# Performance work log

Measured on AMD Instinct MI355X. Metric: run time of the kernel, lower is better.

## Reference

```python
import jax, jax.numpy as jnp
import numpy as np

NUM_HEADS = 16
D_MODEL = 1024
DK = D_MODEL // NUM_HEADS


def setup_inputs() -> dict:
    key = jax.random.key(0)
    kH, kq, kk, kv, ko = jax.random.split(key, 5)
    scale = 0.02
    return {
        "H": jax.random.normal(kH, (4, 2048, D_MODEL), dtype=jnp.float32),
        "Wq": jax.random.normal(kq, (D_MODEL, D_MODEL), dtype=jnp.float32) * scale,
        "Wk": jax.random.normal(kk, (D_MODEL, D_MODEL), dtype=jnp.float32) * scale,
        "Wv": jax.random.normal(kv, (D_MODEL, D_MODEL), dtype=jnp.float32) * scale,
        "Wo": jax.random.normal(ko, (D_MODEL, D_MODEL), dtype=jnp.float32) * scale,
    }


def reference(H, Wq, Wk, Wv, Wo):
    b, T, d = H.shape
    n, dk = NUM_HEADS, DK
    # projections -> [b, n, T, dk]
    def split_heads(x):
        return x.reshape(b, T, n, dk).transpose(0, 2, 1, 3)
    Q = split_heads(H @ Wq)
    K = split_heads(H @ Wk)
    V = split_heads(H @ Wv)
    scores = jnp.einsum("bntd,bnsd->bnts", Q, K) / jnp.sqrt(jnp.float32(dk))
    causal = jnp.tril(jnp.ones((T, T), dtype=bool))
    scores = jnp.where(causal[None, None], scores, -jnp.inf)
    attn = jax.nn.softmax(scores, axis=-1)  # dropout rate 0 -> identity
    out = jnp.einsum("bnts,bnsd->bntd", attn, V)  # [b, n, T, dk]
    out = out.transpose(0, 2, 1, 3).reshape(b, T, n * dk)
    return out @ Wo
```

## Files before the change

### kernel.cpp

```cpp
#include <hip/hip_runtime.h>
#include <hip/hip_bf16.h>

#define T_SEQ 2048
#define DM 1024
#define DM2 2048
#define NH 16
#define DKH 64
#define NBATCH 4
#define MROWS (NBATCH*T_SEQ)

typedef __attribute__((ext_vector_type(8))) short bf16x8;
typedef __attribute__((ext_vector_type(4))) short bf16x4;
typedef __attribute__((ext_vector_type(4))) float f32x4;
typedef __attribute__((ext_vector_type(4))) unsigned short u16x4;

#define NEG_INF (-__builtin_inff())

#if __has_builtin(__builtin_amdgcn_exp2f)
#define EXP2(x) __builtin_amdgcn_exp2f(x)
#else
#define EXP2(x) exp2f(x)
#endif

static __device__ __forceinline__ unsigned short f2bf(float f){
  union { float f; unsigned u; } v; v.f = f;
  unsigned r = v.u + 0x7fffu + ((v.u >> 16) & 1u);
  return (unsigned short)(r >> 16);
}

static __device__ __forceinline__ unsigned short f2bfc(float f){
  union { __hip_bfloat16 h; unsigned short u; } cv;
  cv.h = __float2bfloat16(f);
  return cv.u;
}

static __device__ __forceinline__ void gload_lds16(const void* g, void* l){
  __builtin_amdgcn_global_load_lds(
      (const __attribute__((address_space(1))) void*)g,
      (__attribute__((address_space(3))) void*)l, 16, 0, 0);
}

__global__ __launch_bounds__(256) void convprep(
    const float* __restrict__ H,
    const float* __restrict__ W0, const float* __restrict__ W1,
    const float* __restrict__ W2, const float* __restrict__ W3,
    u16x4* __restrict__ Hb4,
    unsigned short* __restrict__ O0, unsigned short* __restrict__ O1,
    unsigned short* __restrict__ O2, unsigned short* __restrict__ O3)
{
  __shared__ float t[32][33];
  const int bid = blockIdx.x, tid = threadIdx.x;
  if (bid < 4096){
    const int z = bid >> 10, rem = bid & 1023;
    const int nx = (rem & 31)*32, kx = (rem >> 5)*32;
    const float* W = (z==0)?W0:(z==1)?W1:(z==2)?W2:W3;
    unsigned short* O = (z==0)?O0:(z==1)?O1:(z==2)?O2:O3;
    const float sc = (z==0) ? 0.18033688f : 1.0f;
    const int tx = tid & 31, ty = tid >> 5;
    #pragma unroll
    for (int i = 0; i < 4; ++i)
      t[ty + i*8][tx] = W[(size_t)(kx + ty + i*8)*DM + nx + tx];
    __syncthreads();
    #pragma unroll
    for (int i = 0; i < 4; ++i)
      O[(size_t)(nx + ty + i*8)*DM + kx + tx] = f2bf(t[tx][ty + i*8] * sc);
  } else {
    const int n4 = MROWS*DM/4;
    for (int i = (bid - 4096)*256 + tid; i < n4; i += 2048*256){
      float4 v = ((const float4*)H)[i];
      u16x4 o;
      o[0] = f2bf(v.x); o[1] = f2bf(v.y); o[2] = f2bf(v.z); o[3] = f2bf(v.w);
      Hb4[i] = o;
    }
  }
}

template<bool F32OUT>
static __device__ __forceinline__ void gemm_body(
    const unsigned short* __restrict__ A, const unsigned short* __restrict__ Bt,
    void* __restrict__ Cp, int N, int K, int m0, int n0,
    unsigned short* a_lds, unsigned short* b_lds)
{
  const int tid = threadIdx.x;
  const int w = tid >> 6, l = tid & 63;
  const int g = l >> 4, lr = l & 15;
  const int wr = w >> 1, wc = w & 1;
  f32x4 acc[4][4] = {};
  const int nk = K >> 6;
  for (int ks = 0; ks < nk; ++ks){
    __syncthreads();
    const int k0 = ks << 6;
    #pragma unroll
    for (int i = 0; i < 4; ++i){
      int c = (w*4 + i)*64 + l;
      int row = c >> 3;
      int gc = (c & 7) ^ (row & 7);
      gload_lds16(A + (size_t)(m0 + row)*K + (k0 + gc*8), &a_lds[c*8]);
    }
    #pragma unroll
    for (int i = 0; i < 4; ++i){
      int c = (w*4 + i)*64 + l;
      int row = c >> 3;
      int gc = (c & 7) ^ (row & 7);
      gload_lds16(Bt + (size_t)(n0 + row)*K + (k0 + gc*8), &b_lds[c*8]);
    }
    __syncthreads();
    #pragma unroll
    for (int kc = 0; kc < 2; ++kc){
      bf16x8 af[4], bf_[4];
      #pragma unroll
      for (int mt = 0; mt < 4; ++mt){
        int row = wr*64 + mt*16 + lr;
        int off = row*128 + ((kc*64 + g*16) ^ ((row & 7) << 4));
        af[mt] = *(const bf16x8*)((const char*)a_lds + off);
      }
      #pragma unroll
      for (int nt = 0; nt < 4; ++nt){
        int row = wc*64 + nt*16 + lr;
        int off = row*128 + ((kc*64 + g*16) ^ ((row & 7) << 4));
        bf_[nt] = *(const bf16x8*)((const char*)b_lds + off);
      }
      #pragma unroll
      for (int mt = 0; mt < 4; ++mt)
        #pragma unroll
        for (int nt = 0; nt < 4; ++nt)
          acc[mt][nt] = __builtin_amdgcn_mfma_f32_16x16x32_bf16(af[mt], bf_[nt], acc[mt][nt], 0, 0, 0);
    }
  }
  #pragma unroll
  for (int mt = 0; mt < 4; ++mt){
    #pragma unroll
    for (int nt = 0; nt < 4; ++nt){
      const int col = n0 + wc*64 + nt*16 + lr;
      #pragma unroll
      for (int r = 0; r < 4; ++r){
        const int row = m0 + wr*64 + mt*16 + 4*g + r;
        if (F32OUT) ((float*)Cp)[(size_t)row*N + col] = acc[mt][nt][r];
        else ((unsigned short*)Cp)[(size_t)row*N + col] = f2bf(acc[mt][nt][r]);
      }
    }
  }
}

__global__ __launch_bounds__(256) void gemm_qkv(
    const unsigned short* __restrict__ Hb, const unsigned short* __restrict__ Wqkt,
    unsigned short* __restrict__ QKb,
    const unsigned short* __restrict__ Wvt, unsigned short* __restrict__ Vtb)
{
  __shared__ __attribute__((aligned(16))) unsigned short a_lds[128*64];
  __shared__ __attribute__((aligned(16))) unsigned short b_lds[128*64];
  const int bid = blockIdx.x;
  const unsigned short *A, *Bt; unsigned short* Cp; int N, m0, n0;
  if (bid < 1024){
    A = Hb; Bt = Wqkt; Cp = QKb; N = DM2;
    m0 = (bid & 63)*128; n0 = (bid >> 6)*128;
  } else {
    const int t2 = bid - 1024;
    A = Wvt; Bt = Hb; Cp = Vtb; N = MROWS;
    m0 = (t2 & 7)*128; n0 = (t2 >> 3)*128;
  }
  gemm_body<false>(A, Bt, Cp, N, DM, m0, n0, a_lds, b_lds);
}

__global__ __launch_bounds__(256) void gemm_out(
    const unsigned short* __restrict__ Ab, const unsigned short* __restrict__ Wot,
    float* __restrict__ Out)
{
  __shared__ __attribute__((aligned(16))) unsigned short a_lds[128*64];
  __shared__ __attribute__((aligned(16))) unsigned short b_lds[128*64];
  gemm_body<true>(Ab, Wot, Out, DM, DM, blockIdx.x*128, blockIdx.y*128, a_lds, b_lds);
}

static __device__ __forceinline__ void softmax_tile8(
    f32x4 (&s)[8], float& m_run, f32x4 (&acc)[5],
    bf16x4 (&pb)[8], int j0, int qg, int g, bool fullTile)
{
  if (!fullTile){
    #pragma unroll
    for (int kc = 0; kc < 8; ++kc)
      #pragma unroll
      for (int r = 0; r < 4; ++r){
        int kvg = j0 + kc*16 + 4*g + r;
        s[kc][r] = (kvg <= qg) ? s[kc][r] : NEG_INF;
      }
  }
  float m4[8];
  #pragma unroll
  for (int kc = 0; kc < 8; ++kc)
    m4[kc] = fmaxf(fmaxf(s[kc][0], s[kc][1]), fmaxf(s[kc][2], s[kc][3]));
  float tm = fmaxf(fmaxf(fmaxf(m4[0], m4[1]), fmaxf(m4[2], m4[3])),
                   fmaxf(fmaxf(m4[4], m4[5]), fmaxf(m4[6], m4[7])));
  tm = fmaxf(tm, __shfl_xor(tm, 16));
  tm = fmaxf(tm, __shfl_xor(tm, 32));
  float mm;
  if (__all(tm - m_run <= 8.f)){
    mm = m_run;
  } else {
    const float m_new = fmaxf(m_run, tm);
    const float fac = EXP2(m_run - m_new);
    m_run = m_new; mm = m_new;
    #pragma unroll
    for (int mt = 0; mt < 5; ++mt){
      acc[mt][0] *= fac; acc[mt][1] *= fac; acc[mt][2] *= fac; acc[mt][3] *= fac;
    }
  }
  #pragma unroll
  for (int kc = 0; kc < 8; ++kc){
    float e0 = EXP2(s[kc][0] - mm); float e1 = EXP2(s[kc][1] - mm);
    float e2 = EXP2(s[kc][2] - mm); float e3 = EXP2(s[kc][3] - mm);
    bf16x4 t;
    t[0] = (short)f2bfc(e0); t[1] = (short)f2bfc(e1);
    t[2] = (short)f2bfc(e2); t[3] = (short)f2bfc(e3);
    pb[kc] = t;
  }
}

__global__ __launch_bounds__(512, 4) void attn_kernel(const unsigned short* __restrict__ QK,
                                                      const unsigned short* __restrict__ Vt,
                                                      unsigned short* __restrict__ Og)
{
  __shared__ __attribute__((aligned(16))) unsigned short k_lds[2][128*64];
  __shared__ __attribute__((aligned(16))) unsigned short v_lds[2][64*128];
  const int tid = threadIdx.x;
  const int w = tid >> 6, l = tid & 63;
  const int g = l >> 4, lr = l & 15;
  const int L = blockIdx.x;
  const int xcd = L & 7, idx = L >> 3;
  const int bh = xcd*8 + (idx & 7);
  const int pair = idx >> 3;
  const int b = bh >> 4, h = bh & 15;
  const size_t baseK = (size_t)(b*T_SEQ)*DM2 + 1024 + h*DKH;
  const size_t baseV = (size_t)(h*DKH)*MROWS + (size_t)b*T_SEQ;
  const bf16x4 vone = {(short)0x3F80, (short)0x3F80, (short)0x3F80, (short)0x3F80};

  const int cA = tid, cB = tid + 512;
  const int krA = cA >> 3, kgA = (cA & 7) ^ (krA & 7);
  const int krB = cB >> 3, kgB = (cB & 7) ^ (krB & 7);
  const int vrA = cA >> 4, vgA = (cA & 15) ^ (vrA & 15);
  const int vrB = cB >> 4, vgB = (cB & 15) ^ (vrB & 15);

  auto STAGE = [&](int jt, int buf){
    const int j0s = jt * 128;
    gload_lds16(QK + baseK + (size_t)(j0s + krA)*DM2 + kgA*8, &k_lds[buf][cA*8]);
    gload_lds16(QK + baseK + (size_t)(j0s + krB)*DM2 + kgB*8, &k_lds[buf][cB*8]);
    gload_lds16(Vt + baseV + (size_t)vrA*MROWS + j0s + vgA*8, &v_lds[buf][cA*8]);
    gload_lds16(Vt + baseV + (size_t)vrB*MROWS + j0s + vgB*8, &v_lds[buf][cB*8]);
  };

#define ROUND(JT, CUR) do{                                                       \
    const int jt_ = (JT);                                                        \
    if (jt_ + 1 < ntiles) STAGE(jt_ + 1, (CUR)^1);                               \
    const int j0_ = jt_ * 128;                                                   \
    f32x4 s[8];                                                                  \
    __builtin_amdgcn_s_setprio(1);                                               \
    _Pragma("unroll")                                                            \
    for (int kc = 0; kc < 8; ++kc){                                              \
      f32x4 z = {};                                                              \
      _Pragma("unroll")                                                          \
      for (int c2 = 0; c2 < 2; ++c2){                                            \
        int row = kc*16 + lr;                                                    \
        int off = row*128 + ((c2*64 + g*16) ^ ((row & 7) << 4));                 \
        bf16x8 kf = *(const bf16x8*)((const char*)k_lds[CUR] + off);             \
        z = __builtin_amdgcn_mfma_f32_16x16x32_bf16(kf, qf[c2], z, 0, 0, 0);     \
      }                                                                          \
      s[kc] = z;                                                                 \
    }                                                                            \
    __builtin_amdgcn_s_setprio(0);                                               \
    bf16x4 pb[8];                                                                \
    softmax_tile8(s, m_run, acc, pb, j0_, qg, g, jt_ < qblk);                    \
    __builtin_amdgcn_s_setprio(1);                                               \
    _Pragma("unroll")                                                            \
    for (int mt = 0; mt < 4; ++mt){                                              \
      const int vrow = mt*16 + lr;                                               \
      _Pragma("unroll")                                                          \
      for (int kc = 0; kc < 8; ++kc){                                            \
        const int voff = vrow*256 + ((((kc<<1) + (g>>1)) ^ (vrow & 15)) << 4)    \
                         + ((g & 1) << 3);                                       \
        bf16x4 vf = *(const bf16x4*)((const char*)v_lds[CUR] + voff);            \
        acc[mt] = __builtin_amdgcn_mfma_f32_16x16x16bf16_1k(vf, pb[kc], acc[mt], 0, 0, 0); \
      }                                                                          \
    }                                                                            \
    _Pragma("unroll")                                                            \
    for (int kc = 0; kc < 8; ++kc)                                               \
      acc[4] = __builtin_amdgcn_mfma_f32_16x16x16bf16_1k(vone, pb[kc], acc[4], 0, 0, 0); \
    __builtin_amdgcn_s_setprio(0);                                               \
    __syncthreads();                                                             \
  } while(0)

  #pragma unroll 1
  for (int seg = 0; seg < 2; ++seg){
    const int qblk = seg ? pair : (15 - pair);
    const int q0 = qblk * 128;
    const int qg = q0 + w*16 + lr;
    const size_t rowQ = (size_t)(b*T_SEQ + qg)*DM2 + h*DKH;
    bf16x8 qf[2];
    qf[0] = *(const bf16x8*)(QK + rowQ + g*8);
    qf[1] = *(const bf16x8*)(QK + rowQ + 32 + g*8);
    float m_run = NEG_INF;
    f32x4 acc[5] = {};
    const int ntiles = qblk + 1;

    STAGE(0, 0);
    __syncthreads();

    int jt = 0;
    #pragma unroll 1
    for (; jt + 2 <= ntiles; jt += 2){
      ROUND(jt, 0);
      ROUND(jt + 1, 1);
    }
    if (jt < ntiles) ROUND(jt, 0);

    const float inv = 1.f / acc[4][0];
    const size_t rowO = (size_t)(b*T_SEQ + qg)*DM + h*DKH;
    #pragma unroll
    for (int mt = 0; mt < 4; ++mt){
      unsigned u0 = (unsigned)f2bfc(acc[mt][0]*inv) | ((unsigned)f2bfc(acc[mt][1]*inv) << 16);
      unsigned u1 = (unsigned)f2bfc(acc[mt][2]*inv) | ((unsigned)f2bfc(acc[mt][3]*inv) << 16);
      *(unsigned*)(Og + rowO + mt*16 + 4*g)     = u0;
      *(unsigned*)(Og + rowO + mt*16 + 4*g + 2) = u1;
    }
  }
#undef ROUND
}

extern "C" void kernel_launch(void* const* d_in, const int* in_sizes, int n_in,
                              void* d_out, int out_size, void* d_ws, size_t ws_size,
                              hipStream_t stream)
{
  (void)in_sizes; (void)n_in; (void)out_size; (void)ws_size;
  const float* H  = (const float*)d_in[0];
  const float* Wq = (const float*)d_in[1];
  const float* Wk = (const float*)d_in[2];
  const float* Wv = (const float*)d_in[3];
  const float* Wo = (const float*)d_in[4];
  char* ws = (char*)d_ws;
  unsigned short* Hb   = (unsigned short*)(ws);
  unsigned short* Wqkt = (unsigned short*)(ws + 16777216);
  unsigned short* Wkt  = (unsigned short*)(ws + 18874368);
  unsigned short* Wvt  = (unsigned short*)(ws + 20971520);
  unsigned short* Wot  = (unsigned short*)(ws + 23068672);
  unsigned short* QKb  = (unsigned short*)(ws + 25165824);
  unsigned short* Vtb  = (unsigned short*)(ws + 58720256);
  unsigned short* Ab   = (unsigned short*)(ws + 75497472);

  convprep<<<6144, 256, 0, stream>>>(H, Wq, Wk, Wv, Wo,
                                     (u16x4*)Hb, Wqkt, Wkt, Wvt, Wot);
  gemm_qkv<<<1536, 256, 0, stream>>>(Hb, Wqkt, QKb, Wvt, Vtb);
  attn_kernel<<<dim3(512), 512, 0, stream>>>(QKb, Vtb, Ab);
  gemm_out<<<dim3(64,8), 256, 0, stream>>>(Ab, Wot, (float*)d_out);
}
```

Baseline: 171.2 us.

## Rewrite attention kernel with 32x32 MFMA tiles and 256-row query blocks

Switches the attention kernel from 16x16 MFMA tiles to 32x32x16 bf16 MFMA. Each wave now owns 32 query rows and each block covers 256 query rows, so the grid halves to 256 blocks and launch bounds drop to 2 blocks per CU. The row sum is now kept in a scalar accumulator instead of an extra ones-vector MFMA, and causal half-tiles beyond a wave's rows are skipped. K rows are permuted at staging time to match the 32x32 output layout. The goal is fewer MFMA and LDS instructions per FLOP, at the cost of lower occupancy, a smaller grid, and more register pressure.

```diff
diff --git a/kernel.cpp b/kernel.cpp
--- a/kernel.cpp
+++ b/kernel.cpp
@@ -12,6 +12,7 @@
 typedef __attribute__((ext_vector_type(8))) short bf16x8;
 typedef __attribute__((ext_vector_type(4))) short bf16x4;
 typedef __attribute__((ext_vector_type(4))) float f32x4;
+typedef __attribute__((ext_vector_type(16))) float f32x16;
 typedef __attribute__((ext_vector_type(4))) unsigned short u16x4;
 
 #define NEG_INF (-__builtin_inff())
@@ -21,6 +22,8 @@
 #else
 #define EXP2(x) exp2f(x)
 #endif
+
+#define MFMA32(A,B,C) __builtin_amdgcn_mfma_f32_32x32x16_bf16(A,B,C,0,0,0)
 
 static __device__ __forceinline__ unsigned short f2bf(float f){
   union { float f; unsigned u; } v; v.f = f;
@@ -171,51 +174,60 @@
   gemm_body<true>(Ab, Wot, Out, DM, DM, blockIdx.x*128, blockIdx.y*128, a_lds, b_lds);
 }
 
-static __device__ __forceinline__ void softmax_tile8(
-    f32x4 (&s)[8], float& m_run, f32x4 (&acc)[5],
-    bf16x4 (&pb)[8], int j0, int qg, int g, bool fullTile)
-{
-  if (!fullTile){
-    #pragma unroll
-    for (int kc = 0; kc < 8; ++kc)
-      #pragma unroll
-      for (int r = 0; r < 4; ++r){
-        int kvg = j0 + kc*16 + 4*g + r;
-        s[kc][r] = (kvg <= qg) ? s[kc][r] : NEG_INF;
-      }
-  }
-  float m4[8];
+static __device__ __forceinline__ void half_softmax(
+    f32x16& st0, f32x16& st1, float& m_run, float& l_run,
+    f32x16& acc0, f32x16& acc1, bf16x8 (&pb)[4],
+    int kvb, int qg, bool fullT)
+{
+  if (!fullT){
+    #pragma unroll
+    for (int r = 0; r < 16; ++r){
+      const int kvo = (r & 3) + 4*((r >> 2) & 1) + 16*(r >> 3);
+      st0[r] = (kvb + kvo      <= qg) ? st0[r] : NEG_INF;
+      st1[r] = (kvb + 32 + kvo <= qg) ? st1[r] : NEG_INF;
+    }
+  }
+  float m01[8];
   #pragma unroll
-  for (int kc = 0; kc < 8; ++kc)
-    m4[kc] = fmaxf(fmaxf(s[kc][0], s[kc][1]), fmaxf(s[kc][2], s[kc][3]));
-  float tm = fmaxf(fmaxf(fmaxf(m4[0], m4[1]), fmaxf(m4[2], m4[3])),
-                   fmaxf(fmaxf(m4[4], m4[5]), fmaxf(m4[6], m4[7])));
-  tm = fmaxf(tm, __shfl_xor(tm, 16));
-  tm = fmaxf(tm, __shfl_xor(tm, 32));
-  float mm;
-  if (__all(tm - m_run <= 8.f)){
-    mm = m_run;
-  } else {
-    const float m_new = fmaxf(m_run, tm);
-    const float fac = EXP2(m_run - m_new);
-    m_run = m_new; mm = m_new;
-    #pragma unroll
-    for (int mt = 0; mt < 5; ++mt){
-      acc[mt][0] *= fac; acc[mt][1] *= fac; acc[mt][2] *= fac; acc[mt][3] *= fac;
-    }
-  }
+  for (int r = 0; r < 8; ++r)
+    m01[r] = fmaxf(fmaxf(st0[2*r], st0[2*r+1]), fmaxf(st1[2*r], st1[2*r+1]));
+  float tm = fmaxf(fmaxf(fmaxf(m01[0],m01[1]), fmaxf(m01[2],m01[3])),
+                   fmaxf(fmaxf(m01[4],m01[5]), fmaxf(m01[6],m01[7])));
+  float mm = m_run;
+  if (!__all(tm - m_run <= 8.f)){
+    float tg = fmaxf(tm, __shfl_xor(tm, 32));
+    const float mn = fmaxf(m_run, tg);
+    const float fac = EXP2(m_run - mn);
+    l_run *= fac;
+    #pragma unroll
+    for (int r = 0; r < 16; ++r){ acc0[r] *= fac; acc1[r] *= fac; }
+    m_run = mn; mm = mn;
+  }
+  float ps0 = 0.f, ps1 = 0.f, ps2 = 0.f, ps3 = 0.f;
   #pragma unroll
-  for (int kc = 0; kc < 8; ++kc){
-    float e0 = EXP2(s[kc][0] - mm); float e1 = EXP2(s[kc][1] - mm);
-    float e2 = EXP2(s[kc][2] - mm); float e3 = EXP2(s[kc][3] - mm);
-    bf16x4 t;
-    t[0] = (short)f2bfc(e0); t[1] = (short)f2bfc(e1);
-    t[2] = (short)f2bfc(e2); t[3] = (short)f2bfc(e3);
-    pb[kc] = t;
-  }
-}
-
-__global__ __launch_bounds__(512, 4) void attn_kernel(const unsigned short* __restrict__ QK,
+  for (int r = 0; r < 4; ++r){
+    float e0 = EXP2(st0[4*r+0]-mm), e1 = EXP2(st0[4*r+1]-mm);
+    float e2 = EXP2(st0[4*r+2]-mm), e3 = EXP2(st0[4*r+3]-mm);
+    float f0 = EXP2(st1[4*r+0]-mm), f1 = EXP2(st1[4*r+1]-mm);
+    float f2 = EXP2(st1[4*r+2]-mm), f3 = EXP2(st1[4*r+3]-mm);
+    ps0 += e0 + f0; ps1 += e1 + f1; ps2 += e2 + f2; ps3 += e3 + f3;
+    st0[4*r+0]=e0; st0[4*r+1]=e1; st0[4*r+2]=e2; st0[4*r+3]=e3;
+    st1[4*r+0]=f0; st1[4*r+1]=f1; st1[4*r+2]=f2; st1[4*r+3]=f3;
+  }
+  l_run += (ps0 + ps1) + (ps2 + ps3);
+  #pragma unroll
+  for (int m = 0; m < 2; ++m){
+    bf16x8 t0, t1;
+    #pragma unroll
+    for (int i = 0; i < 8; ++i){
+      t0[i] = (short)f2bfc(st0[8*m+i]);
+      t1[i] = (short)f2bfc(st1[8*m+i]);
+    }
+    pb[m] = t0; pb[2+m] = t1;
+  }
+}
+
+__global__ __launch_bounds__(512, 2) void attn_kernel(const unsigned short* __restrict__ QK,
                                                       const unsigned short* __restrict__ Vt,
                                                       unsigned short* __restrict__ Og)
 {
@@ -223,7 +235,7 @@
   __shared__ __attribute__((aligned(16))) unsigned short v_lds[2][64*128];
   const int tid = threadIdx.x;
   const int w = tid >> 6, l = tid & 63;
-  const int g = l >> 4, lr = l & 15;
+  const int h1 = l >> 5, lq = l & 31;
   const int L = blockIdx.x;
   const int xcd = L & 7, idx = L >> 3;
   const int bh = xcd*8 + (idx & 7);
@@ -231,94 +243,97 @@
   const int b = bh >> 4, h = bh & 15;
   const size_t baseK = (size_t)(b*T_SEQ)*DM2 + 1024 + h*DKH;
   const size_t baseV = (size_t)(h*DKH)*MROWS + (size_t)b*T_SEQ;
-  const bf16x4 vone = {(short)0x3F80, (short)0x3F80, (short)0x3F80, (short)0x3F80};
 
   const int cA = tid, cB = tid + 512;
-  const int krA = cA >> 3, kgA = (cA & 7) ^ (krA & 7);
-  const int krB = cB >> 3, kgB = (cB & 7) ^ (krB & 7);
+  const int krA = cA >> 3, krB = cB >> 3;
+  const int kiA = (cA & 7) ^ (krA & 7), kiB = (cB & 7) ^ (krB & 7);
+  const int kvA = 32*(krA >> 5) + 16*((krA >> 4) & 1) + 8*((krA >> 2) & 1) + 4*((krA >> 3) & 1) + (krA & 3);
+  const int kvB = 32*(krB >> 5) + 16*((krB >> 4) & 1) + 8*((krB >> 2) & 1) + 4*((krB >> 3) & 1) + (krB & 3);
   const int vrA = cA >> 4, vgA = (cA & 15) ^ (vrA & 15);
   const int vrB = cB >> 4, vgB = (cB & 15) ^ (vrB & 15);
 
   auto STAGE = [&](int jt, int buf){
     const int j0s = jt * 128;
-    gload_lds16(QK + baseK + (size_t)(j0s + krA)*DM2 + kgA*8, &k_lds[buf][cA*8]);
-    gload_lds16(QK + baseK + (size_t)(j0s + krB)*DM2 + kgB*8, &k_lds[buf][cB*8]);
+    gload_lds16(QK + baseK + (size_t)(j0s + kvA)*DM2 + kiA*8, &k_lds[buf][cA*8]);
+    gload_lds16(QK + baseK + (size_t)(j0s + kvB)*DM2 + kiB*8, &k_lds[buf][cB*8]);
     gload_lds16(Vt + baseV + (size_t)vrA*MROWS + j0s + vgA*8, &v_lds[buf][cA*8]);
     gload_lds16(Vt + baseV + (size_t)vrB*MROWS + j0s + vgB*8, &v_lds[buf][cB*8]);
   };
 
-#define ROUND(JT, CUR) do{                                                       \
-    const int jt_ = (JT);                                                        \
-    if (jt_ + 1 < ntiles) STAGE(jt_ + 1, (CUR)^1);                               \
-    const int j0_ = jt_ * 128;                                                   \
-    f32x4 s[8];                                                                  \
-    __builtin_amdgcn_s_setprio(1);                                               \
-    _Pragma("unroll")                                                            \
-    for (int kc = 0; kc < 8; ++kc){                                              \
-      f32x4 z = {};                                                              \
-      _Pragma("unroll")                                                          \
-      for (int c2 = 0; c2 < 2; ++c2){                                            \
-        int row = kc*16 + lr;                                                    \
-        int off = row*128 + ((c2*64 + g*16) ^ ((row & 7) << 4));                 \
-        bf16x8 kf = *(const bf16x8*)((const char*)k_lds[CUR] + off);             \
-        z = __builtin_amdgcn_mfma_f32_16x16x32_bf16(kf, qf[c2], z, 0, 0, 0);     \
-      }                                                                          \
-      s[kc] = z;                                                                 \
-    }                                                                            \
-    __builtin_amdgcn_s_setprio(0);                                               \
-    bf16x4 pb[8];                                                                \
-    softmax_tile8(s, m_run, acc, pb, j0_, qg, g, jt_ < qblk);                    \
-    __builtin_amdgcn_s_setprio(1);                                               \
-    _Pragma("unroll")                                                            \
-    for (int mt = 0; mt < 4; ++mt){                                              \
-      const int vrow = mt*16 + lr;                                               \
-      _Pragma("unroll")                                                          \
-      for (int kc = 0; kc < 8; ++kc){                                            \
-        const int voff = vrow*256 + ((((kc<<1) + (g>>1)) ^ (vrow & 15)) << 4)    \
-                         + ((g & 1) << 3);                                       \
-        bf16x4 vf = *(const bf16x4*)((const char*)v_lds[CUR] + voff);            \
-        acc[mt] = __builtin_amdgcn_mfma_f32_16x16x16bf16_1k(vf, pb[kc], acc[mt], 0, 0, 0); \
-      }                                                                          \
-    }                                                                            \
-    _Pragma("unroll")                                                            \
-    for (int kc = 0; kc < 8; ++kc)                                               \
-      acc[4] = __builtin_amdgcn_mfma_f32_16x16x16bf16_1k(vone, pb[kc], acc[4], 0, 0, 0); \
-    __builtin_amdgcn_s_setprio(0);                                               \
-    __syncthreads();                                                             \
+#define ROUND(JT, CUR) do{                                                        \
+    const int jt_ = (JT);                                                         \
+    if (jt_ + 1 < ntiles) STAGE(jt_ + 1, (CUR)^1);                                \
+    const int j0_ = jt_ * 128;                                                    \
+    _Pragma("unroll")                                                             \
+    for (int h2 = 0; h2 < 2; ++h2){                                               \
+      if (j0_ + 64*h2 <= qhi){                                                    \
+        f32x16 st0 = {}, st1 = {};                                                \
+        __builtin_amdgcn_s_setprio(1);                                            \
+        _Pragma("unroll")                                                         \
+        for (int s = 0; s < 4; ++s){                                              \
+          const int r0_ = 64*h2 + lq, r1_ = r0_ + 32;                             \
+          bf16x8 kf0 = *(const bf16x8*)((const char*)k_lds[CUR] + r0_*128 + (((2*s + h1) ^ (r0_ & 7)) << 4)); \
+          bf16x8 kf1 = *(const bf16x8*)((const char*)k_lds[CUR] + r1_*128 + (((2*s + h1) ^ (r1_ & 7)) << 4)); \
+          st0 = MFMA32(kf0, qf[s], st0);                                          \
+          st1 = MFMA32(kf1, qf[s], st1);                                          \
+        }                                                                         \
+        __builtin_amdgcn_s_setprio(0);                                            \
+        bf16x8 pb[4];                                                             \
+        half_softmax(st0, st1, m_run, l_run, acc0, acc1, pb,                      \
+                     j0_ + 64*h2 + 8*h1, qg, (j0_ + 64*h2 + 63) <= qlo);          \
+        __builtin_amdgcn_s_setprio(1);                                            \
+        _Pragma("unroll")                                                         \
+        for (int jl = 0; jl < 4; ++jl){                                           \
+          const int vr0 = lq, vr1 = 32 + lq;                                      \
+          bf16x8 vf0 = *(const bf16x8*)((const char*)v_lds[CUR] + vr0*256 + (((2*(4*h2 + jl) + h1) ^ (vr0 & 15)) << 4)); \
+          bf16x8 vf1 = *(const bf16x8*)((const char*)v_lds[CUR] + vr1*256 + (((2*(4*h2 + jl) + h1) ^ (vr1 & 15)) << 4)); \
+          acc0 = MFMA32(vf0, pb[jl], acc0);                                       \
+          acc1 = MFMA32(vf1, pb[jl], acc1);                                       \
+        }                                                                         \
+        __builtin_amdgcn_s_setprio(0);                                            \
+      }                                                                           \
+    }                                                                             \
+    __syncthreads();                                                              \
   } while(0)
 
   #pragma unroll 1
   for (int seg = 0; seg < 2; ++seg){
-    const int qblk = seg ? pair : (15 - pair);
-    const int q0 = qblk * 128;
-    const int qg = q0 + w*16 + lr;
+    const int qblk = seg ? pair : (7 - pair);
+    const int q0 = qblk * 256;
+    const int qlo = q0 + 32*w;
+    const int qhi = qlo + 31;
+    const int qg = qlo + lq;
     const size_t rowQ = (size_t)(b*T_SEQ + qg)*DM2 + h*DKH;
-    bf16x8 qf[2];
-    qf[0] = *(const bf16x8*)(QK + rowQ + g*8);
-    qf[1] = *(const bf16x8*)(QK + rowQ + 32 + g*8);
-    float m_run = NEG_INF;
-    f32x4 acc[5] = {};
-    const int ntiles = qblk + 1;
+    bf16x8 qf[4];
+    #pragma unroll
+    for (int s = 0; s < 4; ++s)
+      qf[s] = *(const bf16x8*)(QK + rowQ + 16*s + 8*h1);
+    float m_run = NEG_INF, l_run = 0.f;
+    f32x16 acc0 = {}, acc1 = {};
+    const int ntiles = 2*qblk + 2;
 
     STAGE(0, 0);
     __syncthreads();
 
-    int jt = 0;
     #pragma unroll 1
-    for (; jt + 2 <= ntiles; jt += 2){
+    for (int jt = 0; jt < ntiles; jt += 2){
       ROUND(jt, 0);
       ROUND(jt + 1, 1);
     }
-    if (jt < ntiles) ROUND(jt, 0);
-
-    const float inv = 1.f / acc[4][0];
+
+    const float ls = l_run + __shfl_xor(l_run, 32);
+    const float inv = 1.f / ls;
     const size_t rowO = (size_t)(b*T_SEQ + qg)*DM + h*DKH;
     #pragma unroll
-    for (int mt = 0; mt < 4; ++mt){
-      unsigned u0 = (unsigned)f2bfc(acc[mt][0]*inv) | ((unsigned)f2bfc(acc[mt][1]*inv) << 16);
-      unsigned u1 = (unsigned)f2bfc(acc[mt][2]*inv) | ((unsigned)f2bfc(acc[mt][3]*inv) << 16);
-      *(unsigned*)(Og + rowO + mt*16 + 4*g)     = u0;
-      *(unsigned*)(Og + rowO + mt*16 + 4*g + 2) = u1;
+    for (int d = 0; d < 2; ++d){
+      const f32x16& A = d ? acc1 : acc0;
+      #pragma unroll
+      for (int bb = 0; bb < 4; ++bb){
+        unsigned u0 = (unsigned)f2bfc(A[4*bb+0]*inv) | ((unsigned)f2bfc(A[4*bb+1]*inv) << 16);
+        unsigned u1 = (unsigned)f2bfc(A[4*bb+2]*inv) | ((unsigned)f2bfc(A[4*bb+3]*inv) << 16);
+        uint2 uv; uv.x = u0; uv.y = u1;
+        *(uint2*)(Og + rowO + 32*d + 8*bb + 4*h1) = uv;
+      }
     }
   }
 #undef ROUND
@@ -347,6 +362,6 @@
   convprep<<<6144, 256, 0, stream>>>(H, Wq, Wk, Wv, Wo,
                                      (u16x4*)Hb, Wqkt, Wkt, Wvt, Wot);
   gemm_qkv<<<1536, 256, 0, stream>>>(Hb, Wqkt, QKb, Wvt, Vtb);
-  attn_kernel<<<dim3(512), 512, 0, stream>>>(QKb, Vtb, Ab);
+  attn_kernel<<<dim3(256), 512, 0, stream>>>(QKb, Vtb, Ab);
   gemm_out<<<dim3(64,8), 256, 0, stream>>>(Ab, Wot, (float*)d_out);
 }
```

New measurement: 154.2 us. 9.9% less time.
